# Optimization experiments

Hardware: AMD Instinct MI355X
Metric: run time of the kernel (lower is better)

The kernel has to match this reference:

```python
import jax, jax.numpy as jnp
import numpy as np

NUM_Q = 8
K = 1024          # codebook_size
D = 256           # latent_dim
N = 65536         # number of vectors
COMMIT = 0.25


def setup_inputs() -> dict:
    key = jax.random.key(0)
    kz, kc = jax.random.split(key)
    z = jax.random.normal(kz, (N, D), dtype=jnp.float32)
    # torch init: uniform(-1/K, 1/K) per quantizer
    codebooks = jax.random.uniform(kc, (NUM_Q, K, D), dtype=jnp.float32,
                                   minval=-1.0 / K, maxval=1.0 / K)
    return {"z": z, "codebooks": codebooks}


def _vq_step(residual, W):
    # residual: [N, D], W: [K, D]
    # squared L2 distances [N, K] (same expansion as the torch code)
    d = (jnp.sum(residual ** 2, axis=1, keepdims=True)
         + jnp.sum(W ** 2, axis=1)
         - 2.0 * residual @ W.T)
    idx = jnp.argmin(d, axis=1)                      # [N]
    zq = W[idx]                                      # gather == one-hot @ W
    zq_ste = residual + jax.lax.stop_gradient(zq - residual)
    commitment = jnp.mean((jax.lax.stop_gradient(residual) - zq) ** 2)
    codebook_l = jnp.mean((residual - jax.lax.stop_gradient(zq)) ** 2)
    loss = codebook_l + COMMIT * commitment
    return zq_ste, idx, loss


def reference(z, codebooks):
    def step(residual, W):
        zq_ste, idx, loss = _vq_step(residual, W)
        residual_new = residual - jax.lax.stop_gradient(zq_ste)
        return residual_new, (zq_ste, idx, loss)

    _, (all_q, all_idx, losses) = jax.lax.scan(step, z, codebooks)
    z_reconstructed = jnp.sum(all_q, axis=0)          # [N, D]
    final_indices = all_idx.T[:, :, None]             # [N, Q, 1] (torch stacks [N,1] on dim=1)
    total_loss = jnp.sum(losses)
    return z_reconstructed, final_indices, total_loss
```

## Files before the change

### kernel.cpp

```cpp
#include <hip/hip_runtime.h>
#include <stdint.h>


#define NQ      8
#define KCODES  1024
#define DIM     256
#define NVEC    65536
#define ROWS    64
#define CCH     16
#define NCH     (KCODES / CCH)
#define WARM    8
#define CAP     24

typedef unsigned int u32;
typedef unsigned long long u64;
typedef unsigned short u16;
typedef short bf16x8 __attribute__((ext_vector_type(8)));
typedef float f32x4  __attribute__((ext_vector_type(4)));

__device__ float  g_norms[NQ * KCODES];
__device__ u32    g_nkmax;
__device__ double g_loss;
__device__ __align__(16) u16 g_wb[(size_t)NQ * KCODES * DIM];
__device__ float  g_resid[(size_t)NVEC * DIM];

__device__ __forceinline__ u16 bf16rne(float x){
    u32 u = __float_as_uint(x);
    return (u16)((u + 0x7FFFu + ((u >> 16) & 1u)) >> 16);
}

__device__ __forceinline__ u64 pack4(float4 v){
    return  (u64)bf16rne(v.x)        | ((u64)bf16rne(v.y) << 16)
         | ((u64)bf16rne(v.z) << 32) | ((u64)bf16rne(v.w) << 48);
}

__device__ __forceinline__ void gload_lds16(const void* g, void* l){
    __builtin_amdgcn_global_load_lds(
        (const __attribute__((address_space(1))) u32*)g,
        (__attribute__((address_space(3))) u32*)l, 16, 0, 0);
}

__device__ __forceinline__ float np_sumsq128(const float* __restrict__ a){
    float r0,r1,r2,r3,r4,r5,r6,r7;
    {
        float4 v0 = *(const float4*)(a);
        float4 v1 = *(const float4*)(a + 4);
        r0 = __fmul_rn(v0.x,v0.x); r1 = __fmul_rn(v0.y,v0.y);
        r2 = __fmul_rn(v0.z,v0.z); r3 = __fmul_rn(v0.w,v0.w);
        r4 = __fmul_rn(v1.x,v1.x); r5 = __fmul_rn(v1.y,v1.y);
        r6 = __fmul_rn(v1.z,v1.z); r7 = __fmul_rn(v1.w,v1.w);
    }
    for (int i = 8; i < 128; i += 8){
        float4 v0 = *(const float4*)(a + i);
        float4 v1 = *(const float4*)(a + i + 4);
        r0 = __fadd_rn(r0, __fmul_rn(v0.x,v0.x));
        r1 = __fadd_rn(r1, __fmul_rn(v0.y,v0.y));
        r2 = __fadd_rn(r2, __fmul_rn(v0.z,v0.z));
        r3 = __fadd_rn(r3, __fmul_rn(v0.w,v0.w));
        r4 = __fadd_rn(r4, __fmul_rn(v1.x,v1.x));
        r5 = __fadd_rn(r5, __fmul_rn(v1.y,v1.y));
        r6 = __fadd_rn(r6, __fmul_rn(v1.z,v1.z));
        r7 = __fadd_rn(r7, __fmul_rn(v1.w,v1.w));
    }
    return __fadd_rn(__fadd_rn(__fadd_rn(r0,r1), __fadd_rn(r2,r3)),
                     __fadd_rn(__fadd_rn(r4,r5), __fadd_rn(r6,r7)));
}

__global__ void vq_zero(){ g_loss = 0.0; g_nkmax = 0u; }

__global__ void vq_norms_np(const float* __restrict__ cb){
    int row = blockIdx.x * 256 + threadIdx.x;
    const float* a = cb + (size_t)row * DIM;
    float n = __fadd_rn(np_sumsq128(a), np_sumsq128(a + 128));
    g_norms[row] = n;
    atomicMax(&g_nkmax, __float_as_uint(n));
}

__global__ void vq_prep_wb(const float* __restrict__ cb){
    int t = blockIdx.x * 256 + threadIdx.x;
    int code = t >> 5, s = t & 31;
    const float* src = cb + (size_t)code * DIM + s * 8;
    float4 v0 = *(const float4*)(src);
    float4 v1 = *(const float4*)(src + 4);
    u64* dst = (u64*)(g_wb + (size_t)code * DIM + ((s ^ (code & 7)) << 3));
    dst[0] = pack4(v0); dst[1] = pack4(v1);
}

__device__ __forceinline__ void ldsAtomicMinU64(u64* p, u64 v){
    u64 old = *p;
    while (v < old){
        u64 a = old;
        old = atomicCAS(p, a, v);
        if (old == a) break;
    }
}

__global__ __launch_bounds__(256, 4)
void vq_main(const float* __restrict__ z, const float* __restrict__ cb,
             float* __restrict__ out)
{
    __shared__ __align__(16) u16 Wst[2][CCH * DIM];
    __shared__ float nt[KCODES];
    __shared__ float t1[ROWS];
    __shared__ u32   rminU[ROWS];
    __shared__ u32   cnt[ROWS];
    __shared__ u16   cand[ROWS * CAP];
    __shared__ u64   bestKey[ROWS];
    __shared__ int   off[ROWS + 1];
    __shared__ int   totalS, ovf;

    const int tid     = threadIdx.x;
    const int rowbase = blockIdx.x * ROWS;
    const int w       = tid >> 6;
    const int lane    = tid & 63;
    const int l15     = lane & 15, lg = lane >> 4;
    const int key     = l15 & 7;
    const int urow    = tid >> 2, us = tid & 3;
    double lossAcc = 0.0;

    const float sqnkmax = sqrtf(__uint_as_float(g_nkmax));

    for (int q = 0; q < NQ; ++q){
        const float* rsrc = q ? (const float*)g_resid : z;
        const char*  wbq  = (const char*)g_wb + (size_t)q * KCODES * DIM * 2;

        {
            char* d = (char*)Wst[0];
#pragma unroll
            for (int r = 0; r < 2; ++r){
                int o = (r * 256 + tid) * 16;
                gload_lds16(wbq + o, d + o);
            }
        }
        *(float4*)(nt + tid * 4) = *(const float4*)(g_norms + q * KCODES + tid * 4);
        if (tid < 128){
            float s = np_sumsq128(rsrc + (size_t)(rowbase + (tid >> 1)) * DIM
                                  + (tid & 1) * 128);
            float o = __shfl_xor(s, 1);
            if (!(tid & 1)) t1[tid >> 1] = __fadd_rn(s, o);
        }
        if (tid < ROWS){
            rminU[tid]   = 0x7f800000u;
            cnt[tid]     = 0u;
            bestKey[tid] = ~0ull;
        }
        bf16x8 a[8];
        {
            const float* rr = rsrc + (size_t)(rowbase + w * 16 + l15) * DIM + lg * 8;
#pragma unroll
            for (int ks = 0; ks < 8; ++ks){
                float4 v0 = *(const float4*)(rr + ks * 32);
                float4 v1 = *(const float4*)(rr + ks * 32 + 4);
                union { bf16x8 v; u64 p[2]; } u;
                u.p[0] = pack4(v0); u.p[1] = pack4(v1);
                a[ks] = u.v;
            }
        }
        __syncthreads();
        if (tid == 0 && q > 0)
            for (int r = 0; r < ROWS; ++r) lossAcc += (double)t1[r];

        float t1r[4], delta[4], mloc[4], thr[4];
#pragma unroll
        for (int j = 0; j < 4; ++j){
            t1r[j]   = t1[w * 16 + lg * 4 + j];
            delta[j] = 0.02f * sqrtf(t1r[j]) * sqnkmax + 3e-4f;
            mloc[j]  = __int_as_float(0x7f800000);
            thr[j]   = -1.0f;
        }

        for (int tt = 0; tt < NCH + WARM; ++tt){
            int  cc      = (tt < NCH) ? tt : (tt - NCH);
            int  cur     = tt & 1;
            bool collect = (tt >= WARM);

            if (tt && (tt & 3) == 0){
#pragma unroll
                for (int j = 0; j < 4; ++j){
                    float g = __uint_as_float(rminU[w * 16 + lg * 4 + j]);
                    thr[j] = fminf(g, mloc[j]) + delta[j];
                }
            }
            if (tt + 1 < NCH + WARM){
                int nc = (tt + 1 < NCH) ? tt + 1 : (tt + 1 - NCH);
                const char* src = wbq + (size_t)nc * (CCH * DIM * 2);
                char* d = (char*)Wst[cur ^ 1];
#pragma unroll
                for (int r = 0; r < 2; ++r){
                    int o = (r * 256 + tid) * 16;
                    gload_lds16(src + o, d + o);
                }
            }

            float nk = nt[cc * CCH + l15];
            const u16* wrow = Wst[cur] + l15 * DIM;
            f32x4 acc = {0.f, 0.f, 0.f, 0.f};
#pragma unroll
            for (int ks = 0; ks < 8; ++ks){
                bf16x8 b = *(const bf16x8*)(wrow + (((ks * 4 + lg) ^ key) << 3));
                acc = __builtin_amdgcn_mfma_f32_16x16x32_bf16(a[ks], b, acc, 0, 0, 0);
            }
            int codeg = cc * CCH + l15;
#pragma unroll
            for (int j = 0; j < 4; ++j){
                float dest = (t1r[j] + nk) - 2.0f * acc[j];
                mloc[j] = fminf(mloc[j], dest);
                if (collect && dest <= thr[j]){
                    int row = w * 16 + lg * 4 + j;
                    u32 slot = atomicAdd(&cnt[row], 1u);
                    if (slot < CAP) cand[row * CAP + slot] = (u16)codeg;
                }
            }
            if ((tt & 3) == 3){
                float m[4];
#pragma unroll
                for (int j = 0; j < 4; ++j) m[j] = mloc[j];
#pragma unroll
                for (int msk = 1; msk < 16; msk <<= 1)
#pragma unroll
                    for (int j = 0; j < 4; ++j)
                        m[j] = fminf(m[j], __shfl_xor(m[j], msk));
                if (l15 == 0){
#pragma unroll
                    for (int j = 0; j < 4; ++j)
                        atomicMin(&rminU[w * 16 + lg * 4 + j],
                                  __float_as_uint(m[j]));
                }
            }
            __syncthreads();
        }

        if (tid < 64){
            int c    = min((int)cnt[tid], CAP);
            int over = cnt[tid] > CAP;
            int x = c;
#pragma unroll
            for (int o = 1; o < 64; o <<= 1){
                int y = __shfl_up(x, o);
                if (tid >= o) x += y;
            }
            off[tid] = x - c;
            if (tid == 63){ off[64] = x; totalS = x; }
#pragma unroll
            for (int o = 1; o < 64; o <<= 1) over |= __shfl_xor(over, o);
            if (tid == 0) ovf = over;
        }
        __syncthreads();

        int nT = totalS;
        for (int t = tid; t < nT; t += 256){
            int r = 0;
            while (off[r + 1] <= t) ++r;
            int k = (int)cand[r * CAP + (t - off[r])];
            const float* wr = cb + ((size_t)q * KCODES + k) * DIM;
            const float* rr = rsrc + (size_t)(rowbase + r) * DIM;
            float dot = 0.f;
#pragma unroll 4
            for (int i = 0; i < 64; ++i){
                float4 rv = *(const float4*)(rr + i * 4);
                float4 wv = *(const float4*)(wr + i * 4);
                dot = __builtin_fmaf(rv.x, wv.x, dot);
                dot = __builtin_fmaf(rv.y, wv.y, dot);
                dot = __builtin_fmaf(rv.z, wv.z, dot);
                dot = __builtin_fmaf(rv.w, wv.w, dot);
            }
            float d = __fsub_rn(__fadd_rn(t1[r], nt[k]), __fmul_rn(2.0f, dot));
            ldsAtomicMinU64(&bestKey[r], ((u64)__float_as_uint(d) << 32) | (u32)k);
        }
        if (ovf){
            for (int r = 0; r < ROWS; ++r){
                if (cnt[r] > CAP){
                    for (int k = tid; k < KCODES; k += 256){
                        const float* wr = cb + ((size_t)q * KCODES + k) * DIM;
                        const float* rr = rsrc + (size_t)(rowbase + r) * DIM;
                        float dot = 0.f;
                        for (int i = 0; i < 64; ++i){
                            float4 rv = *(const float4*)(rr + i * 4);
                            float4 wv = *(const float4*)(wr + i * 4);
                            dot = __builtin_fmaf(rv.x, wv.x, dot);
                            dot = __builtin_fmaf(rv.y, wv.y, dot);
                            dot = __builtin_fmaf(rv.z, wv.z, dot);
                            dot = __builtin_fmaf(rv.w, wv.w, dot);
                        }
                        float d = __fsub_rn(__fadd_rn(t1[r], nt[k]),
                                            __fmul_rn(2.0f, dot));
                        ldsAtomicMinU64(&bestKey[r], ((u64)__float_as_uint(d) << 32) | (u32)k);
                    }
                }
            }
        }
        __syncthreads();

        if (tid < ROWS)
            out[(size_t)NVEC * DIM + (size_t)(rowbase + tid) * NQ + q] =
                (float)(int)(bestKey[tid] & 0xFFFFFFFFull);

        {
            int k = (int)(bestKey[urow] & 0xFFFFFFFFull);
            const float* wrow = cb + ((size_t)q * KCODES + k) * DIM;
            const float* rrow = rsrc + (size_t)(rowbase + urow) * DIM;
            float*       grow = g_resid + (size_t)(rowbase + urow) * DIM;
#pragma unroll
            for (int j = 0; j < 16; ++j){
                int d0 = us * 4 + j * 16;
                float4 r4 = *(const float4*)(rrow + d0);
                float4 wv = *(const float4*)(wrow + d0);
                float4 rn;
                rn.x = __fsub_rn(r4.x, __fadd_rn(r4.x, __fsub_rn(wv.x, r4.x)));
                rn.y = __fsub_rn(r4.y, __fadd_rn(r4.y, __fsub_rn(wv.y, r4.y)));
                rn.z = __fsub_rn(r4.z, __fadd_rn(r4.z, __fsub_rn(wv.z, r4.z)));
                rn.w = __fsub_rn(r4.w, __fadd_rn(r4.w, __fsub_rn(wv.w, r4.w)));
                *(float4*)(grow + d0) = rn;
            }
        }
        __syncthreads();
    }

    if (tid < 128){
        float s = np_sumsq128(g_resid + (size_t)(rowbase + (tid >> 1)) * DIM
                              + (tid & 1) * 128);
        float o = __shfl_xor(s, 1);
        if (!(tid & 1)) t1[tid >> 1] = __fadd_rn(s, o);
    }
    __syncthreads();
    if (tid == 0){
        for (int r = 0; r < ROWS; ++r) lossAcc += (double)t1[r];
        atomicAdd(&g_loss, lossAcc);
    }

#pragma unroll
    for (int l = 0; l < 16; ++l){
        int i = l * 256 + tid;
        int row = i >> 6, c4 = i & 63;
        size_t base = (size_t)(rowbase + row) * DIM + c4 * 4;
        float4 zv = *(const float4*)(z + base);
        float4 rv = *(const float4*)(g_resid + base);
        float4 ov;
        ov.x = __fsub_rn(zv.x, rv.x);
        ov.y = __fsub_rn(zv.y, rv.y);
        ov.z = __fsub_rn(zv.z, rv.z);
        ov.w = __fsub_rn(zv.w, rv.w);
        *(float4*)(out + base) = ov;
    }
}

__global__ void vq_loss_final(float* __restrict__ out){
    if (threadIdx.x == 0 && blockIdx.x == 0){
        double m = 1.25 * g_loss / ((double)NVEC * (double)DIM);
        out[(size_t)NVEC * DIM + (size_t)NVEC * NQ] = (float)m;
    }
}

extern "C" void kernel_launch(void* const* d_in, const int* in_sizes, int n_in,
                              void* d_out, int out_size, void* d_ws, size_t ws_size,
                              hipStream_t stream) {
    (void)in_sizes; (void)n_in; (void)out_size; (void)d_ws; (void)ws_size;
    const float* z  = (const float*)d_in[0];
    const float* cb = (const float*)d_in[1];
    float* out = (float*)d_out;

    hipLaunchKernelGGL(vq_zero,       dim3(1),    dim3(1),   0, stream);
    hipLaunchKernelGGL(vq_norms_np,   dim3(32),   dim3(256), 0, stream, cb);
    hipLaunchKernelGGL(vq_prep_wb,    dim3(1024), dim3(256), 0, stream, cb);
    hipLaunchKernelGGL(vq_main,       dim3(NVEC / ROWS), dim3(256), 0, stream, z, cb, out);
    hipLaunchKernelGGL(vq_loss_final, dim3(1),    dim3(64),  0, stream, out);
}
```

Measured before the change: 1.261 ms.

## Widen code chunks, fuse residual update with norms and output, prefetch next codebook

Doubles the codebook chunk to 32 codes per iteration, with two MFMAs per k-step sharing the A fragment. The warmup pass shrinks and the threshold refresh now runs every two chunks. The residual update now also computes the next row norms, writes a bf16 copy of the residual for the next stage's A fragments, and on the last stage writes the reconstruction directly. This removes the separate norm pass and the final epilogue. It also prefetches the next quantizer's first chunk during the update, replaces the linear row search with a task-row table, and reads code norms from global memory instead of LDS. In exchange it uses a larger LDS stage, lowers the candidate cap (more overflow fallbacks), and adds extra global writes for the bf16 residual.

```diff
diff --git a/kernel.cpp b/kernel.cpp
--- a/kernel.cpp
+++ b/kernel.cpp
@@ -7,10 +7,11 @@
 #define DIM     256
 #define NVEC    65536
 #define ROWS    64
-#define CCH     16
+#define CCH     32
 #define NCH     (KCODES / CCH)
-#define WARM    8
-#define CAP     24
+#define WARM    2
+#define NITER   (NCH + WARM)
+#define CAP     16
 
 typedef unsigned int u32;
 typedef unsigned long long u64;
@@ -23,6 +24,7 @@
 __device__ double g_loss;
 __device__ __align__(16) u16 g_wb[(size_t)NQ * KCODES * DIM];
 __device__ float  g_resid[(size_t)NVEC * DIM];
+__device__ __align__(16) u16 g_residb[(size_t)NVEC * DIM];
 
 __device__ __forceinline__ u16 bf16rne(float x){
     u32 u = __float_as_uint(x);
@@ -100,11 +102,11 @@
              float* __restrict__ out)
 {
     __shared__ __align__(16) u16 Wst[2][CCH * DIM];
-    __shared__ float nt[KCODES];
     __shared__ float t1[ROWS];
     __shared__ u32   rminU[ROWS];
     __shared__ u32   cnt[ROWS];
     __shared__ u16   cand[ROWS * CAP];
+    __shared__ u16   taskRow[ROWS * CAP];
     __shared__ u64   bestKey[ROWS];
     __shared__ int   off[ROWS + 1];
     __shared__ int   totalS, ovf;
@@ -115,50 +117,47 @@
     const int lane    = tid & 63;
     const int l15     = lane & 15, lg = lane >> 4;
     const int key     = l15 & 7;
-    const int urow    = tid >> 2, us = tid & 3;
     double lossAcc = 0.0;
 
     const float sqnkmax = sqrtf(__uint_as_float(g_nkmax));
+
+    {
+        char* d = (char*)Wst[0];
+#pragma unroll
+        for (int r = 0; r < 4; ++r){
+            int o = (r * 256 + tid) * 16;
+            gload_lds16((const char*)g_wb + o, d + o);
+        }
+    }
+    if (tid < 128){
+        float s = np_sumsq128(z + (size_t)(rowbase + (tid >> 1)) * DIM
+                              + (tid & 1) * 128);
+        float o = __shfl_xor(s, 1);
+        if (!(tid & 1)) t1[tid >> 1] = __fadd_rn(s, o);
+    }
+    if (tid < ROWS){
+        rminU[tid]   = 0x7f800000u;
+        cnt[tid]     = 0u;
+        bestKey[tid] = ~0ull;
+    }
+    bf16x8 a[8];
+    {
+        const float* rr = z + (size_t)(rowbase + w * 16 + l15) * DIM + lg * 8;
+#pragma unroll
+        for (int ks = 0; ks < 8; ++ks){
+            float4 v0 = *(const float4*)(rr + ks * 32);
+            float4 v1 = *(const float4*)(rr + ks * 32 + 4);
+            union { bf16x8 v; u64 p[2]; } u;
+            u.p[0] = pack4(v0); u.p[1] = pack4(v1);
+            a[ks] = u.v;
+        }
+    }
+    __syncthreads();
 
     for (int q = 0; q < NQ; ++q){
         const float* rsrc = q ? (const float*)g_resid : z;
         const char*  wbq  = (const char*)g_wb + (size_t)q * KCODES * DIM * 2;
-
-        {
-            char* d = (char*)Wst[0];
-#pragma unroll
-            for (int r = 0; r < 2; ++r){
-                int o = (r * 256 + tid) * 16;
-                gload_lds16(wbq + o, d + o);
-            }
-        }
-        *(float4*)(nt + tid * 4) = *(const float4*)(g_norms + q * KCODES + tid * 4);
-        if (tid < 128){
-            float s = np_sumsq128(rsrc + (size_t)(rowbase + (tid >> 1)) * DIM
-                                  + (tid & 1) * 128);
-            float o = __shfl_xor(s, 1);
-            if (!(tid & 1)) t1[tid >> 1] = __fadd_rn(s, o);
-        }
-        if (tid < ROWS){
-            rminU[tid]   = 0x7f800000u;
-            cnt[tid]     = 0u;
-            bestKey[tid] = ~0ull;
-        }
-        bf16x8 a[8];
-        {
-            const float* rr = rsrc + (size_t)(rowbase + w * 16 + l15) * DIM + lg * 8;
-#pragma unroll
-            for (int ks = 0; ks < 8; ++ks){
-                float4 v0 = *(const float4*)(rr + ks * 32);
-                float4 v1 = *(const float4*)(rr + ks * 32 + 4);
-                union { bf16x8 v; u64 p[2]; } u;
-                u.p[0] = pack4(v0); u.p[1] = pack4(v1);
-                a[ks] = u.v;
-            }
-        }
-        __syncthreads();
-        if (tid == 0 && q > 0)
-            for (int r = 0; r < ROWS; ++r) lossAcc += (double)t1[r];
+        const float* nrm  = g_norms + q * KCODES;
 
         float t1r[4], delta[4], mloc[4], thr[4];
 #pragma unroll
@@ -169,49 +168,60 @@
             thr[j]   = -1.0f;
         }
 
-        for (int tt = 0; tt < NCH + WARM; ++tt){
+        for (int tt = 0; tt < NITER; ++tt){
             int  cc      = (tt < NCH) ? tt : (tt - NCH);
             int  cur     = tt & 1;
             bool collect = (tt >= WARM);
 
-            if (tt && (tt & 3) == 0){
+            if (tt >= 2 && (tt & 1) == 0){
 #pragma unroll
                 for (int j = 0; j < 4; ++j){
                     float g = __uint_as_float(rminU[w * 16 + lg * 4 + j]);
                     thr[j] = fminf(g, mloc[j]) + delta[j];
                 }
             }
-            if (tt + 1 < NCH + WARM){
+            if (tt + 1 < NITER){
                 int nc = (tt + 1 < NCH) ? tt + 1 : (tt + 1 - NCH);
                 const char* src = wbq + (size_t)nc * (CCH * DIM * 2);
                 char* d = (char*)Wst[cur ^ 1];
 #pragma unroll
-                for (int r = 0; r < 2; ++r){
+                for (int r = 0; r < 4; ++r){
                     int o = (r * 256 + tid) * 16;
                     gload_lds16(src + o, d + o);
                 }
             }
 
-            float nk = nt[cc * CCH + l15];
-            const u16* wrow = Wst[cur] + l15 * DIM;
-            f32x4 acc = {0.f, 0.f, 0.f, 0.f};
+            const u16* w0 = Wst[cur] + l15 * DIM;
+            const u16* w1 = Wst[cur] + (16 + l15) * DIM;
+            f32x4 acc0 = {0,0,0,0}, acc1 = {0,0,0,0};
 #pragma unroll
             for (int ks = 0; ks < 8; ++ks){
-                bf16x8 b = *(const bf16x8*)(wrow + (((ks * 4 + lg) ^ key) << 3));
-                acc = __builtin_amdgcn_mfma_f32_16x16x32_bf16(a[ks], b, acc, 0, 0, 0);
-            }
-            int codeg = cc * CCH + l15;
+                int so = ((ks * 4 + lg) ^ key) << 3;
+                bf16x8 b0 = *(const bf16x8*)(w0 + so);
+                bf16x8 b1 = *(const bf16x8*)(w1 + so);
+                acc0 = __builtin_amdgcn_mfma_f32_16x16x32_bf16(a[ks], b0, acc0, 0, 0, 0);
+                acc1 = __builtin_amdgcn_mfma_f32_16x16x32_bf16(a[ks], b1, acc1, 0, 0, 0);
+            }
+            float nk0 = nrm[cc * CCH + l15];
+            float nk1 = nrm[cc * CCH + 16 + l15];
 #pragma unroll
             for (int j = 0; j < 4; ++j){
-                float dest = (t1r[j] + nk) - 2.0f * acc[j];
-                mloc[j] = fminf(mloc[j], dest);
-                if (collect && dest <= thr[j]){
-                    int row = w * 16 + lg * 4 + j;
-                    u32 slot = atomicAdd(&cnt[row], 1u);
-                    if (slot < CAP) cand[row * CAP + slot] = (u16)codeg;
-                }
-            }
-            if ((tt & 3) == 3){
+                int   row = w * 16 + lg * 4 + j;
+                float d0  = (t1r[j] + nk0) - 2.0f * acc0[j];
+                float d1  = (t1r[j] + nk1) - 2.0f * acc1[j];
+                mloc[j] = fminf(mloc[j], fminf(d0, d1));
+                if (collect){
+                    if (d0 <= thr[j]){
+                        u32 slot = atomicAdd(&cnt[row], 1u);
+                        if (slot < CAP) cand[row * CAP + slot] = (u16)(cc * CCH + l15);
+                    }
+                    if (d1 <= thr[j]){
+                        u32 slot = atomicAdd(&cnt[row], 1u);
+                        if (slot < CAP) cand[row * CAP + slot] = (u16)(cc * CCH + 16 + l15);
+                    }
+                }
+            }
+            if ((tt & 1) == 1){
                 float m[4];
 #pragma unroll
                 for (int j = 0; j < 4; ++j) m[j] = mloc[j];
@@ -246,11 +256,15 @@
             if (tid == 0) ovf = over;
         }
         __syncthreads();
+        if (tid < 64){
+            int b = off[tid], e = off[tid + 1];
+            for (int i = b; i < e; ++i) taskRow[i] = (u16)tid;
+        }
+        __syncthreads();
 
         int nT = totalS;
         for (int t = tid; t < nT; t += 256){
-            int r = 0;
-            while (off[r + 1] <= t) ++r;
+            int r = taskRow[t];
             int k = (int)cand[r * CAP + (t - off[r])];
             const float* wr = cb + ((size_t)q * KCODES + k) * DIM;
             const float* rr = rsrc + (size_t)(rowbase + r) * DIM;
@@ -264,7 +278,7 @@
                 dot = __builtin_fmaf(rv.z, wv.z, dot);
                 dot = __builtin_fmaf(rv.w, wv.w, dot);
             }
-            float d = __fsub_rn(__fadd_rn(t1[r], nt[k]), __fmul_rn(2.0f, dot));
+            float d = __fsub_rn(__fadd_rn(t1[r], nrm[k]), __fmul_rn(2.0f, dot));
             ldsAtomicMinU64(&bestKey[r], ((u64)__float_as_uint(d) << 32) | (u32)k);
         }
         if (ovf){
@@ -282,7 +296,7 @@
                             dot = __builtin_fmaf(rv.z, wv.z, dot);
                             dot = __builtin_fmaf(rv.w, wv.w, dot);
                         }
-                        float d = __fsub_rn(__fadd_rn(t1[r], nt[k]),
+                        float d = __fsub_rn(__fadd_rn(t1[r], nrm[k]),
                                             __fmul_rn(2.0f, dot));
                         ldsAtomicMinU64(&bestKey[r], ((u64)__float_as_uint(d) << 32) | (u32)k);
                     }
@@ -295,53 +309,86 @@
             out[(size_t)NVEC * DIM + (size_t)(rowbase + tid) * NQ + q] =
                 (float)(int)(bestKey[tid] & 0xFFFFFFFFull);
 
-        {
-            int k = (int)(bestKey[urow] & 0xFFFFFFFFull);
-            const float* wrow = cb + ((size_t)q * KCODES + k) * DIM;
-            const float* rrow = rsrc + (size_t)(rowbase + urow) * DIM;
-            float*       grow = g_resid + (size_t)(rowbase + urow) * DIM;
-#pragma unroll
-            for (int j = 0; j < 16; ++j){
-                int d0 = us * 4 + j * 16;
-                float4 r4 = *(const float4*)(rrow + d0);
-                float4 wv = *(const float4*)(wrow + d0);
+        if (q + 1 < NQ){
+            const char* nwbq = wbq + (size_t)KCODES * DIM * 2;
+            char* d = (char*)Wst[0];
+#pragma unroll
+            for (int r = 0; r < 4; ++r){
+                int o = (r * 256 + tid) * 16;
+                gload_lds16(nwbq + o, d + o);
+            }
+        }
+
+        if (tid < 128){
+            int row = tid >> 1, h = tid & 1;
+            int k   = (int)(bestKey[row] & 0xFFFFFFFFull);
+            size_t rb = (size_t)(rowbase + row) * DIM + h * 128;
+            const float* wrow = cb + ((size_t)q * KCODES + k) * DIM + h * 128;
+            const float* rrow = rsrc + rb;
+            float ac[8];
+#pragma unroll 8
+            for (int j = 0; j < 32; ++j){
+                float4 r4 = *(const float4*)(rrow + j * 4);
+                float4 wv = *(const float4*)(wrow + j * 4);
                 float4 rn;
                 rn.x = __fsub_rn(r4.x, __fadd_rn(r4.x, __fsub_rn(wv.x, r4.x)));
                 rn.y = __fsub_rn(r4.y, __fadd_rn(r4.y, __fsub_rn(wv.y, r4.y)));
                 rn.z = __fsub_rn(r4.z, __fadd_rn(r4.z, __fsub_rn(wv.z, r4.z)));
                 rn.w = __fsub_rn(r4.w, __fadd_rn(r4.w, __fsub_rn(wv.w, r4.w)));
-                *(float4*)(grow + d0) = rn;
-            }
+                if (q + 1 < NQ){
+                    *(float4*)(g_resid + rb + j * 4) = rn;
+                    *(u64*)(g_residb + rb + j * 4)   = pack4(rn);
+                } else {
+                    float4 zv = *(const float4*)(z + rb + j * 4);
+                    float4 ov;
+                    ov.x = __fsub_rn(zv.x, rn.x);
+                    ov.y = __fsub_rn(zv.y, rn.y);
+                    ov.z = __fsub_rn(zv.z, rn.z);
+                    ov.w = __fsub_rn(zv.w, rn.w);
+                    *(float4*)(out + rb + j * 4) = ov;
+                }
+                int c0 = (j & 1) * 4;
+                if (j < 2){
+                    ac[c0+0] = __fmul_rn(rn.x, rn.x);
+                    ac[c0+1] = __fmul_rn(rn.y, rn.y);
+                    ac[c0+2] = __fmul_rn(rn.z, rn.z);
+                    ac[c0+3] = __fmul_rn(rn.w, rn.w);
+                } else {
+                    ac[c0+0] = __fadd_rn(ac[c0+0], __fmul_rn(rn.x, rn.x));
+                    ac[c0+1] = __fadd_rn(ac[c0+1], __fmul_rn(rn.y, rn.y));
+                    ac[c0+2] = __fadd_rn(ac[c0+2], __fmul_rn(rn.z, rn.z));
+                    ac[c0+3] = __fadd_rn(ac[c0+3], __fmul_rn(rn.w, rn.w));
+                }
+            }
+            float half = __fadd_rn(__fadd_rn(__fadd_rn(ac[0],ac[1]), __fadd_rn(ac[2],ac[3])),
+                                   __fadd_rn(__fadd_rn(ac[4],ac[5]), __fadd_rn(ac[6],ac[7])));
+            float o = __shfl_xor(half, 1);
+            if (!h) t1[row] = __fadd_rn(half, o);
         }
         __syncthreads();
-    }
-
-    if (tid < 128){
-        float s = np_sumsq128(g_resid + (size_t)(rowbase + (tid >> 1)) * DIM
-                              + (tid & 1) * 128);
-        float o = __shfl_xor(s, 1);
-        if (!(tid & 1)) t1[tid >> 1] = __fadd_rn(s, o);
-    }
-    __syncthreads();
-    if (tid == 0){
-        for (int r = 0; r < ROWS; ++r) lossAcc += (double)t1[r];
-        atomicAdd(&g_loss, lossAcc);
-    }
-
-#pragma unroll
-    for (int l = 0; l < 16; ++l){
-        int i = l * 256 + tid;
-        int row = i >> 6, c4 = i & 63;
-        size_t base = (size_t)(rowbase + row) * DIM + c4 * 4;
-        float4 zv = *(const float4*)(z + base);
-        float4 rv = *(const float4*)(g_resid + base);
-        float4 ov;
-        ov.x = __fsub_rn(zv.x, rv.x);
-        ov.y = __fsub_rn(zv.y, rv.y);
-        ov.z = __fsub_rn(zv.z, rv.z);
-        ov.w = __fsub_rn(zv.w, rv.w);
-        *(float4*)(out + base) = ov;
-    }
+
+        if (tid < 64){
+            float s = t1[tid];
+#pragma unroll
+            for (int o = 1; o < 64; o <<= 1) s += __shfl_xor(s, o);
+            if (tid == 0) lossAcc += (double)s;
+        }
+
+        if (q + 1 < NQ){
+            const u16* rr = g_residb + (size_t)(rowbase + w * 16 + l15) * DIM + lg * 8;
+#pragma unroll
+            for (int ks = 0; ks < 8; ++ks)
+                a[ks] = *(const bf16x8*)(rr + ks * 32);
+            if (tid < ROWS){
+                rminU[tid]   = 0x7f800000u;
+                cnt[tid]     = 0u;
+                bestKey[tid] = ~0ull;
+            }
+        }
+        __syncthreads();
+    }
+
+    if (tid == 0) atomicAdd(&g_loss, lossAcc);
 }
 
 __global__ void vq_loss_final(float* __restrict__ out){
```

Measured after the change: 2.358 ms. 86.9% more time.
